# Kernel optimization log

Measured on AMD Instinct MI355X. Metric: run time of the kernel, lower is better.

The kernel has to match this reference:

```python
import jax, jax.numpy as jnp
import numpy as np

N, E = 50000, 800000
IN_CH, OUT_CH, MSG_DIM, TIME_DIM = 128, 128, 128, 128
HEADS = 2
HEAD_C = OUT_CH // HEADS  # 64
EDGE_DIM = MSG_DIM + TIME_DIM  # 256


def setup_inputs() -> dict:
    key = jax.random.key(0)
    ks = jax.random.split(key, 16)
    s = 0.05
    return {
        "x": jax.random.normal(ks[0], (N, IN_CH), jnp.float32),
        "last_update": jax.random.uniform(ks[1], (N,), jnp.float32),
        "t": jax.random.uniform(ks[2], (E,), jnp.float32),
        "msg": jax.random.normal(ks[3], (E, MSG_DIM), jnp.float32),
        "edge_index": jax.random.randint(ks[4], (2, E), 0, N, jnp.int64),
        # TimeEncoder: Linear(1, TIME_DIM) then cos
        "W_time": jax.random.normal(ks[5], (1, TIME_DIM), jnp.float32) * s,
        "b_time": jax.random.normal(ks[6], (TIME_DIM,), jnp.float32) * s,
        # TransformerConv linears (stored [in, out])
        "Wq": jax.random.normal(ks[7], (IN_CH, OUT_CH), jnp.float32) * s,
        "bq": jax.random.normal(ks[8], (OUT_CH,), jnp.float32) * s,
        "Wk": jax.random.normal(ks[9], (IN_CH, OUT_CH), jnp.float32) * s,
        "bk": jax.random.normal(ks[10], (OUT_CH,), jnp.float32) * s,
        "Wv": jax.random.normal(ks[11], (IN_CH, OUT_CH), jnp.float32) * s,
        "bv": jax.random.normal(ks[12], (OUT_CH,), jnp.float32) * s,
        "We": jax.random.normal(ks[13], (EDGE_DIM, OUT_CH), jnp.float32) * s,  # lin_edge, no bias
        "Ws": jax.random.normal(ks[14], (IN_CH, OUT_CH), jnp.float32) * s,  # lin_skip (root weight)
        "bs": jax.random.normal(ks[15], (OUT_CH,), jnp.float32) * s,
    }


def reference(x, last_update, t, msg, edge_index, W_time, b_time,
              Wq, bq, Wk, bk, Wv, bv, We, Ws, bs):
    src, dst = edge_index[0], edge_index[1]
    # --- temporal edge features ---
    rel_t = last_update[src] - t                      # [E]
    rel_t_enc = jnp.cos(rel_t[:, None] * W_time[0] + b_time)  # [E, TIME_DIM]
    edge_attr = jnp.concatenate([rel_t_enc, msg], axis=-1)    # [E, EDGE_DIM]
    # --- TransformerConv (heads=2, concat=True, root_weight=True, eval: no dropout) ---
    q = (x @ Wq + bq).reshape(N, HEADS, HEAD_C)[dst]   # [E,H,C] query at destination
    k = (x @ Wk + bk).reshape(N, HEADS, HEAD_C)[src]   # [E,H,C] key at source
    v = (x @ Wv + bv).reshape(N, HEADS, HEAD_C)[src]   # [E,H,C]
    e = (edge_attr @ We).reshape(E, HEADS, HEAD_C)     # [E,H,C]
    k = k + e
    alpha = jnp.sum(q * k, axis=-1) / jnp.sqrt(jnp.asarray(HEAD_C, x.dtype))  # [E,H]
    # segment softmax over edges grouped by destination node
    m = jax.ops.segment_max(alpha, dst, num_segments=N)       # [N,H]
    p = jnp.exp(alpha - m[dst])                               # [E,H]
    denom = jax.ops.segment_sum(p, dst, num_segments=N)       # [N,H]
    attn = p / denom[dst]                                     # [E,H]
    out_e = attn[:, :, None] * (v + e)                        # [E,H,C]
    out = jax.ops.segment_sum(out_e, dst, num_segments=N).reshape(N, HEADS * HEAD_C)
    return out + x @ Ws + bs
```

## Files before the change

### kernel.cpp

```cpp
#include <hip/hip_runtime.h>
#include <math.h>

#define N_NODES 50000
#define N_EDGES 800000
#define CH 128
#define GDIM 512

__global__ __launch_bounds__(256) void build_M_kernel(
    const float* __restrict__ Wq, const float* __restrict__ We,
    float* __restrict__ M)
{
    __shared__ float wq[CH];
    const int i = blockIdx.x, t = threadIdx.x;
    if (t < CH) wq[t] = Wq[i * CH + t];
    __syncthreads();
    #pragma unroll
    for (int rep = 0; rep < 2; ++rep) {
        int f  = rep * 256 + t;
        int h  = f >> 8, jj = f & 255;
        const float* wer = We + (size_t)jj * CH + h * 64;
        const float* wqr = wq + h * 64;
        float s = 0.f;
        #pragma unroll 8
        for (int c = 0; c < 64; ++c) s = fmaf(wqr[c], wer[c], s);
        M[(size_t)i * GDIM + f] = s;
    }
}

__global__ void build_gbias_kernel(const float* __restrict__ bq,
                                   const float* __restrict__ We,
                                   float* __restrict__ gb)
{
    int f = blockIdx.x * 256 + threadIdx.x;
    int h = f >> 8, jj = f & 255;
    float s = 0.f;
    #pragma unroll 8
    for (int c = 0; c < 64; ++c)
        s = fmaf(bq[h * 64 + c], We[(size_t)jj * CH + h * 64 + c], s);
    gb[f] = s;
}

__global__ __launch_bounds__(256) void node_linear_kernel(
    const float* __restrict__ x,
    const float* __restrict__ Wq, const float* __restrict__ bq,
    const float* __restrict__ Wk, const float* __restrict__ bk,
    const float* __restrict__ Wv, const float* __restrict__ bv,
    const float* __restrict__ Ws, const float* __restrict__ bs,
    const float* __restrict__ M,  const float* __restrict__ gb,
    float* __restrict__ Q, float* __restrict__ K,
    float* __restrict__ V, float* __restrict__ S, float* __restrict__ G)
{
    __shared__ float xs[64][CH];
    const int t  = threadIdx.x;
    const int n0 = blockIdx.x * 64;

    #pragma unroll
    for (int r = 0; r < 8; ++r) {
        int flat4 = r * 256 + t;
        int row   = flat4 >> 5;
        int c4    = (flat4 & 31) * 4;
        int gr    = n0 + row; if (gr >= N_NODES) gr = N_NODES - 1;
        *(float4*)&xs[row][c4] = *(const float4*)&x[(size_t)gr * CH + c4];
    }
    __syncthreads();

    const int tx = t & 31, ey = t >> 5;
    const int c0 = tx * 4, e0 = ey * 8;

    const float* Wp[8]   = {Wq, Wk, Wv, Ws, M, M + 128, M + 256, M + 384};
    const int    wstr[8] = {CH, CH, CH, CH, GDIM, GDIM, GDIM, GDIM};
    const float* Bp[8]   = {bq, bk, bv, bs, gb, gb + 128, gb + 256, gb + 384};
    float*       Op[8]   = {Q, K, V, S, G, G + 128, G + 256, G + 384};
    const int    ostr[8] = {CH, CH, CH, CH, GDIM, GDIM, GDIM, GDIM};

    #pragma unroll
    for (int m = 0; m < 8; ++m) {
        const float* W = Wp[m];
        const int ws_ = wstr[m];
        float4 acc[8];
        #pragma unroll
        for (int i = 0; i < 8; ++i) acc[i] = make_float4(0.f, 0.f, 0.f, 0.f);
        for (int j = 0; j < CH; ++j) {
            float4 w = *(const float4*)&W[(size_t)j * ws_ + c0];
            #pragma unroll
            for (int i = 0; i < 8; ++i) {
                float a = xs[e0 + i][j];
                acc[i].x = fmaf(a, w.x, acc[i].x);
                acc[i].y = fmaf(a, w.y, acc[i].y);
                acc[i].z = fmaf(a, w.z, acc[i].z);
                acc[i].w = fmaf(a, w.w, acc[i].w);
            }
        }
        float4 b4 = *(const float4*)&Bp[m][c0];
        float* O  = Op[m];
        const int os = ostr[m];
        #pragma unroll
        for (int i = 0; i < 8; ++i) {
            int n = n0 + e0 + i;
            if (n < N_NODES) {
                float4 r = make_float4(acc[i].x + b4.x, acc[i].y + b4.y,
                                       acc[i].z + b4.z, acc[i].w + b4.w);
                *(float4*)&O[(size_t)n * os + c0] = r;
            }
        }
    }
}

__global__ void hist_kernel(const int* __restrict__ ei, int* __restrict__ cnt)
{
    int e = blockIdx.x * 256 + threadIdx.x;
    atomicAdd(&cnt[ei[N_EDGES + e]], 1);
}

__global__ __launch_bounds__(1024) void scan_kernel(
    const int* __restrict__ cnt, int* __restrict__ base, int* __restrict__ cursor)
{
    __shared__ int ssum[1024];
    const int t = threadIdx.x;
    const int STRIP = 49;
    const int s0 = t * STRIP;
    int sum = 0;
    for (int i = 0; i < STRIP; ++i) {
        int idx = s0 + i;
        sum += (idx < N_NODES) ? cnt[idx] : 0;
    }
    ssum[t] = sum;
    __syncthreads();
    for (int off = 1; off < 1024; off <<= 1) {
        int v = (t >= off) ? ssum[t - off] : 0;
        __syncthreads();
        ssum[t] += v;
        __syncthreads();
    }
    int run = (t > 0) ? ssum[t - 1] : 0;
    for (int i = 0; i < STRIP; ++i) {
        int idx = s0 + i;
        if (idx < N_NODES) {
            base[idx] = run; cursor[idx] = run;
            run += cnt[idx];
        }
    }
    if (t == 1023) base[N_NODES] = ssum[1023];
}

__global__ void scatter_kernel(const int* __restrict__ ei,
                               const float* __restrict__ last_update,
                               const float* __restrict__ t_arr,
                               int* __restrict__ cursor,
                               int2* __restrict__ sedge,
                               float* __restrict__ srt)
{
    int e = blockIdx.x * 256 + threadIdx.x;
    int s = ei[e];
    int d = ei[N_EDGES + e];
    int pos = atomicAdd(&cursor[d], 1);
    sedge[pos] = make_int2(s, e);
    srt[pos] = last_update[s] - t_arr[e];
}

__device__ __forceinline__ float wave_allsum(float p) {
    p += __int_as_float(__builtin_amdgcn_update_dpp(
            0, __float_as_int(p), 0xB1, 0xF, 0xF, true));
    p += __int_as_float(__builtin_amdgcn_update_dpp(
            0, __float_as_int(p), 0x4E, 0xF, 0xF, true));
    p += __int_as_float(__builtin_amdgcn_update_dpp(
            0, __float_as_int(p), 0x141, 0xF, 0xF, true));
    p += __int_as_float(__builtin_amdgcn_update_dpp(
            0, __float_as_int(p), 0x140, 0xF, 0xF, true));
    p += __int_as_float(__builtin_amdgcn_ds_swizzle(__float_as_int(p), 0x401F));
    p += __shfl_xor(p, 32);
    return p;
}

__global__ __launch_bounds__(256) void gather_attn_kernel(
    const float* __restrict__ msg,
    const float* __restrict__ W_time,
    const float* __restrict__ b_time,
    const float* __restrict__ We,
    const float* __restrict__ Q, const float* __restrict__ K,
    const float* __restrict__ V, const float* __restrict__ S,
    const float* __restrict__ G,
    const int* __restrict__ base,
    const int2* __restrict__ sedge,
    const float* __restrict__ srt,
    float* __restrict__ out)
{
    __shared__ float wabuf[4][GDIM];
    __shared__ float nvbuf[4][CH];
    __shared__ float dsh[4][2];
    __shared__ int   degsh[4];
    const int wv = threadIdx.x >> 6;
    const int j  = threadIdx.x & 63;
    const int n  = blockIdx.x * 4 + wv;

    const float q0 = Q[(size_t)n * CH + j];
    const float q1 = Q[(size_t)n * CH + 64 + j];
    const float* gn = G + (size_t)n * GDIM + j;
    const float g00 = gn[0],   g01 = gn[64],  g02 = gn[128], g03 = gn[192];
    const float g10 = gn[256], g11 = gn[320], g12 = gn[384], g13 = gn[448];
    const float wt0 = W_time[j], wt1 = W_time[64 + j];
    const float bt0 = b_time[j], bt1 = b_time[64 + j];

    float wa00 = 0.f, wa01 = 0.f, wa02 = 0.f, wa03 = 0.f;
    float wa10 = 0.f, wa11 = 0.f, wa12 = 0.f, wa13 = 0.f;
    float nv0 = 0.f, nv1 = 0.f, den0 = 0.f, den1 = 0.f;

    const int b0 = base[n], b1 = base[n + 1];
    int i = b0;

    for (; i + 2 <= b1; i += 2) {
        const int2  seA = sedge[i];
        const int2  seB = sedge[i + 1];
        const float rtA = srt[i];
        const float rtB = srt[i + 1];
        const float* mA  = msg + (size_t)seA.y * CH;
        const float* mB  = msg + (size_t)seB.y * CH;
        const float* kpA = K   + (size_t)seA.x * CH;
        const float* kpB = K   + (size_t)seB.x * CH;
        const float* vpA = V   + (size_t)seA.x * CH;
        const float* vpB = V   + (size_t)seB.x * CH;

        float ea2A = mA[j],      ea3A = mA[64 + j];
        float ea2B = mB[j],      ea3B = mB[64 + j];
        float k0A  = kpA[j],     k1A  = kpA[64 + j];
        float k0B  = kpB[j],     k1B  = kpB[64 + j];
        float v0A  = vpA[j],     v1A  = vpA[64 + j];
        float v0B  = vpB[j],     v1B  = vpB[64 + j];

        float ea0A = __cosf(fmaf(rtA, wt0, bt0));
        float ea1A = __cosf(fmaf(rtA, wt1, bt1));
        float ea0B = __cosf(fmaf(rtB, wt0, bt0));
        float ea1B = __cosf(fmaf(rtB, wt1, bt1));

        float pA0 = fmaf(q0, k0A, fmaf(ea0A, g00, fmaf(ea1A, g01, fmaf(ea2A, g02, ea3A * g03))));
        float pA1 = fmaf(q1, k1A, fmaf(ea0A, g10, fmaf(ea1A, g11, fmaf(ea2A, g12, ea3A * g13))));
        float pB0 = fmaf(q0, k0B, fmaf(ea0B, g00, fmaf(ea1B, g01, fmaf(ea2B, g02, ea3B * g03))));
        float pB1 = fmaf(q1, k1B, fmaf(ea0B, g10, fmaf(ea1B, g11, fmaf(ea2B, g12, ea3B * g13))));

        pA0 = wave_allsum(pA0);
        pA1 = wave_allsum(pA1);
        pB0 = wave_allsum(pB0);
        pB1 = wave_allsum(pB1);

        pA0 = __expf(pA0 * 0.125f);
        pA1 = __expf(pA1 * 0.125f);
        pB0 = __expf(pB0 * 0.125f);
        pB1 = __expf(pB1 * 0.125f);

        den0 += pA0; den0 += pB0;
        den1 += pA1; den1 += pB1;
        wa00 = fmaf(pA0, ea0A, wa00); wa00 = fmaf(pB0, ea0B, wa00);
        wa01 = fmaf(pA0, ea1A, wa01); wa01 = fmaf(pB0, ea1B, wa01);
        wa02 = fmaf(pA0, ea2A, wa02); wa02 = fmaf(pB0, ea2B, wa02);
        wa03 = fmaf(pA0, ea3A, wa03); wa03 = fmaf(pB0, ea3B, wa03);
        wa10 = fmaf(pA1, ea0A, wa10); wa10 = fmaf(pB1, ea0B, wa10);
        wa11 = fmaf(pA1, ea1A, wa11); wa11 = fmaf(pB1, ea1B, wa11);
        wa12 = fmaf(pA1, ea2A, wa12); wa12 = fmaf(pB1, ea2B, wa12);
        wa13 = fmaf(pA1, ea3A, wa13); wa13 = fmaf(pB1, ea3B, wa13);
        nv0  = fmaf(pA0, v0A, nv0);   nv0  = fmaf(pB0, v0B, nv0);
        nv1  = fmaf(pA1, v1A, nv1);   nv1  = fmaf(pB1, v1B, nv1);
    }

    if (i < b1) {
        const int2  se = sedge[i];
        const float rt = srt[i];
        const float* m  = msg + (size_t)se.y * CH;
        const float* kp = K   + (size_t)se.x * CH;
        const float* vp = V   + (size_t)se.x * CH;
        float ea2 = m[j],  ea3 = m[64 + j];
        float k0  = kp[j], k1  = kp[64 + j];
        float v0  = vp[j], v1  = vp[64 + j];
        float ea0 = __cosf(fmaf(rt, wt0, bt0));
        float ea1 = __cosf(fmaf(rt, wt1, bt1));

        float p0 = fmaf(q0, k0, fmaf(ea0, g00, fmaf(ea1, g01, fmaf(ea2, g02, ea3 * g03))));
        float p1 = fmaf(q1, k1, fmaf(ea0, g10, fmaf(ea1, g11, fmaf(ea2, g12, ea3 * g13))));
        p0 = wave_allsum(p0);
        p1 = wave_allsum(p1);
        p0 = __expf(p0 * 0.125f);
        p1 = __expf(p1 * 0.125f);

        den0 += p0; den1 += p1;
        wa00 = fmaf(p0, ea0, wa00); wa01 = fmaf(p0, ea1, wa01);
        wa02 = fmaf(p0, ea2, wa02); wa03 = fmaf(p0, ea3, wa03);
        wa10 = fmaf(p1, ea0, wa10); wa11 = fmaf(p1, ea1, wa11);
        wa12 = fmaf(p1, ea2, wa12); wa13 = fmaf(p1, ea3, wa13);
        nv0  = fmaf(p0, v0, nv0);
        nv1  = fmaf(p1, v1, nv1);
    }

    wabuf[wv][j]       = wa00; wabuf[wv][64 + j]  = wa01;
    wabuf[wv][128 + j] = wa02; wabuf[wv][192 + j] = wa03;
    wabuf[wv][256 + j] = wa10; wabuf[wv][320 + j] = wa11;
    wabuf[wv][384 + j] = wa12; wabuf[wv][448 + j] = wa13;
    nvbuf[wv][j]      = nv0;
    nvbuf[wv][64 + j] = nv1;
    if (j == 0) {
        dsh[wv][0] = den0; dsh[wv][1] = den1;
        degsh[wv]  = b1 - b0;
    }
    __syncthreads();

    const int col = threadIdx.x & 127;
    const int pr  = threadIdx.x >> 7;
    const int h   = col >> 6;
    const int nA  = 2 * pr, nB = 2 * pr + 1;
    const int wo  = h * 256;

    float aA = 0.f, aB = 0.f;
    #pragma unroll 8
    for (int jj = 0; jj < 256; ++jj) {
        float w = We[(size_t)jj * CH + col];
        aA = fmaf(wabuf[nA][wo + jj], w, aA);
        aB = fmaf(wabuf[nB][wo + jj], w, aB);
    }

    {
        int node = blockIdx.x * 4 + nA;
        float r = (degsh[nA] > 0) ? (nvbuf[nA][col] + aA) / dsh[nA][h] : 0.f;
        out[(size_t)node * CH + col] = r + S[(size_t)node * CH + col];
    }
    {
        int node = blockIdx.x * 4 + nB;
        float r = (degsh[nB] > 0) ? (nvbuf[nB][col] + aB) / dsh[nB][h] : 0.f;
        out[(size_t)node * CH + col] = r + S[(size_t)node * CH + col];
    }
}

extern "C" void kernel_launch(void* const* d_in, const int* in_sizes, int n_in,
                              void* d_out, int out_size, void* d_ws, size_t ws_size,
                              hipStream_t stream) {
    const float* x           = (const float*)d_in[0];
    const float* last_update = (const float*)d_in[1];
    const float* t           = (const float*)d_in[2];
    const float* msg         = (const float*)d_in[3];
    const int*   edge_index  = (const int*)d_in[4];
    const float* W_time      = (const float*)d_in[5];
    const float* b_time      = (const float*)d_in[6];
    const float* Wq = (const float*)d_in[7];
    const float* bq = (const float*)d_in[8];
    const float* Wk = (const float*)d_in[9];
    const float* bk = (const float*)d_in[10];
    const float* Wv = (const float*)d_in[11];
    const float* bv = (const float*)d_in[12];
    const float* We = (const float*)d_in[13];
    const float* Ws = (const float*)d_in[14];
    const float* bs = (const float*)d_in[15];
    float* out = (float*)d_out;

    float* ws = (float*)d_ws;
    const size_t NC = (size_t)N_NODES * CH;
    float* Q  = ws;
    float* K  = Q + NC;
    float* V  = K + NC;
    float* S  = V + NC;
    float* G  = S + NC;
    float* M  = G + (size_t)N_NODES * GDIM;
    float* gb = M + (size_t)CH * GDIM;
    int* cnt    = (int*)(gb + GDIM);
    int* base   = cnt + N_NODES;
    int* cursor = base + N_NODES + 1;
    size_t off = (size_t)((char*)(cursor + N_NODES) - (char*)d_ws);
    off = (off + 7) & ~(size_t)7;
    int2*  sedge = (int2*)((char*)d_ws + off);
    float* srt   = (float*)(sedge + N_EDGES);

    hipMemsetAsync(cnt, 0, (size_t)N_NODES * sizeof(int), stream);

    build_M_kernel<<<CH, 256, 0, stream>>>(Wq, We, M);
    build_gbias_kernel<<<2, 256, 0, stream>>>(bq, We, gb);

    node_linear_kernel<<<(N_NODES + 63) / 64, 256, 0, stream>>>(
        x, Wq, bq, Wk, bk, Wv, bv, Ws, bs, M, gb, Q, K, V, S, G);

    hist_kernel<<<N_EDGES / 256, 256, 0, stream>>>(edge_index, cnt);
    scan_kernel<<<1, 1024, 0, stream>>>(cnt, base, cursor);
    scatter_kernel<<<N_EDGES / 256, 256, 0, stream>>>(
        edge_index, last_update, t, cursor, sedge, srt);

    gather_attn_kernel<<<N_NODES / 4, 256, 0, stream>>>(
        msg, W_time, b_time, We,
        Q, K, V, S, G, base, sedge, srt, out);
}
```

Baseline: 1.167 ms.

## Process four edges per wave with float4 half-wave lanes and packed edge records

Result: slower. 1.217 ms (+4.3%).

```diff
diff --git a/kernel.cpp b/kernel.cpp
--- a/kernel.cpp
+++ b/kernel.cpp
@@ -7,13 +7,16 @@
 #define GDIM 512
 
 __global__ __launch_bounds__(256) void build_M_kernel(
-    const float* __restrict__ Wq, const float* __restrict__ We,
-    float* __restrict__ M)
+    const float* __restrict__ Wq, const float* __restrict__ bq,
+    const float* __restrict__ We,
+    float* __restrict__ M, float* __restrict__ gb)
 {
     __shared__ float wq[CH];
     const int i = blockIdx.x, t = threadIdx.x;
-    if (t < CH) wq[t] = Wq[i * CH + t];
+    const float* srcrow = (i < CH) ? (Wq + (size_t)i * CH) : bq;
+    if (t < CH) wq[t] = srcrow[t];
     __syncthreads();
+    float* orow = (i < CH) ? (M + (size_t)i * GDIM) : gb;
     #pragma unroll
     for (int rep = 0; rep < 2; ++rep) {
         int f  = rep * 256 + t;
@@ -23,21 +26,8 @@
         float s = 0.f;
         #pragma unroll 8
         for (int c = 0; c < 64; ++c) s = fmaf(wqr[c], wer[c], s);
-        M[(size_t)i * GDIM + f] = s;
-    }
-}
-
-__global__ void build_gbias_kernel(const float* __restrict__ bq,
-                                   const float* __restrict__ We,
-                                   float* __restrict__ gb)
-{
-    int f = blockIdx.x * 256 + threadIdx.x;
-    int h = f >> 8, jj = f & 255;
-    float s = 0.f;
-    #pragma unroll 8
-    for (int c = 0; c < 64; ++c)
-        s = fmaf(bq[h * 64 + c], We[(size_t)jj * CH + h * 64 + c], s);
-    gb[f] = s;
+        orow[f] = s;
+    }
 }
 
 __global__ __launch_bounds__(256) void node_linear_kernel(
@@ -147,18 +137,17 @@
                                const float* __restrict__ last_update,
                                const float* __restrict__ t_arr,
                                int* __restrict__ cursor,
-                               int2* __restrict__ sedge,
-                               float* __restrict__ srt)
+                               int4* __restrict__ sedge)
 {
     int e = blockIdx.x * 256 + threadIdx.x;
     int s = ei[e];
     int d = ei[N_EDGES + e];
+    float rt = last_update[s] - t_arr[e];
     int pos = atomicAdd(&cursor[d], 1);
-    sedge[pos] = make_int2(s, e);
-    srt[pos] = last_update[s] - t_arr[e];
-}
-
-__device__ __forceinline__ float wave_allsum(float p) {
+    sedge[pos] = make_int4(s, e, __float_as_int(rt), 0);
+}
+
+__device__ __forceinline__ float half_allsum(float p) {
     p += __int_as_float(__builtin_amdgcn_update_dpp(
             0, __float_as_int(p), 0xB1, 0xF, 0xF, true));
     p += __int_as_float(__builtin_amdgcn_update_dpp(
@@ -168,11 +157,22 @@
     p += __int_as_float(__builtin_amdgcn_update_dpp(
             0, __float_as_int(p), 0x140, 0xF, 0xF, true));
     p += __int_as_float(__builtin_amdgcn_ds_swizzle(__float_as_int(p), 0x401F));
-    p += __shfl_xor(p, 32);
     return p;
 }
 
-__global__ __launch_bounds__(256) void gather_attn_kernel(
+__device__ __forceinline__ float dot4(float4 a, float4 b) {
+    return fmaf(a.x, b.x, fmaf(a.y, b.y, fmaf(a.z, b.z, a.w * b.w)));
+}
+
+#define FMA4(acc, s, v) \
+    acc.x = fmaf(s, v.x, acc.x); acc.y = fmaf(s, v.y, acc.y); \
+    acc.z = fmaf(s, v.z, acc.z); acc.w = fmaf(s, v.w, acc.w)
+
+#define XC4(v) \
+    v.x += __shfl_xor(v.x, 32); v.y += __shfl_xor(v.y, 32); \
+    v.z += __shfl_xor(v.z, 32); v.w += __shfl_xor(v.w, 32)
+
+__global__ __launch_bounds__(256, 4) void gather_attn_kernel(
     const float* __restrict__ msg,
     const float* __restrict__ W_time,
     const float* __restrict__ b_time,
@@ -181,123 +181,111 @@
     const float* __restrict__ V, const float* __restrict__ S,
     const float* __restrict__ G,
     const int* __restrict__ base,
-    const int2* __restrict__ sedge,
-    const float* __restrict__ srt,
+    const int4* __restrict__ sedge,
     float* __restrict__ out)
 {
     __shared__ float wabuf[4][GDIM];
     __shared__ float nvbuf[4][CH];
     __shared__ float dsh[4][2];
     __shared__ int   degsh[4];
-    const int wv = threadIdx.x >> 6;
-    const int j  = threadIdx.x & 63;
-    const int n  = blockIdx.x * 4 + wv;
-
-    const float q0 = Q[(size_t)n * CH + j];
-    const float q1 = Q[(size_t)n * CH + 64 + j];
-    const float* gn = G + (size_t)n * GDIM + j;
-    const float g00 = gn[0],   g01 = gn[64],  g02 = gn[128], g03 = gn[192];
-    const float g10 = gn[256], g11 = gn[320], g12 = gn[384], g13 = gn[448];
-    const float wt0 = W_time[j], wt1 = W_time[64 + j];
-    const float bt0 = b_time[j], bt1 = b_time[64 + j];
-
-    float wa00 = 0.f, wa01 = 0.f, wa02 = 0.f, wa03 = 0.f;
-    float wa10 = 0.f, wa11 = 0.f, wa12 = 0.f, wa13 = 0.f;
-    float nv0 = 0.f, nv1 = 0.f, den0 = 0.f, den1 = 0.f;
+
+    const int wv   = threadIdx.x >> 6;
+    const int lane = threadIdx.x & 63;
+    const int h32  = lane >> 5;
+    const int l    = lane & 31;
+    const int c0   = l * 4;
+    const float mh0 = (l < 16) ? 1.f : 0.f;
+    const int n = blockIdx.x * 4 + wv;
+
+    const float4 q4  = *(const float4*)&Q[(size_t)n * CH + c0];
+    const float* gp  = G + (size_t)n * GDIM;
+    const float4 gt0 = *(const float4*)&gp[c0];
+    const float4 gm0 = *(const float4*)&gp[128 + c0];
+    const float4 gt1 = *(const float4*)&gp[256 + c0];
+    const float4 gm1 = *(const float4*)&gp[384 + c0];
+    const float4 wt4 = *(const float4*)&W_time[c0];
+    const float4 bt4 = *(const float4*)&b_time[c0];
+
+    float4 waT0 = {0,0,0,0}, waM0 = {0,0,0,0};
+    float4 waT1 = {0,0,0,0}, waM1 = {0,0,0,0};
+    float4 nv4  = {0,0,0,0};
+    float den0 = 0.f, den1 = 0.f;
 
     const int b0 = base[n], b1 = base[n + 1];
-    int i = b0;
-
-    for (; i + 2 <= b1; i += 2) {
-        const int2  seA = sedge[i];
-        const int2  seB = sedge[i + 1];
-        const float rtA = srt[i];
-        const float rtB = srt[i + 1];
-        const float* mA  = msg + (size_t)seA.y * CH;
-        const float* mB  = msg + (size_t)seB.y * CH;
-        const float* kpA = K   + (size_t)seA.x * CH;
-        const float* kpB = K   + (size_t)seB.x * CH;
-        const float* vpA = V   + (size_t)seA.x * CH;
-        const float* vpB = V   + (size_t)seB.x * CH;
-
-        float ea2A = mA[j],      ea3A = mA[64 + j];
-        float ea2B = mB[j],      ea3B = mB[64 + j];
-        float k0A  = kpA[j],     k1A  = kpA[64 + j];
-        float k0B  = kpB[j],     k1B  = kpB[64 + j];
-        float v0A  = vpA[j],     v1A  = vpA[64 + j];
-        float v0B  = vpB[j],     v1B  = vpB[64 + j];
-
-        float ea0A = __cosf(fmaf(rtA, wt0, bt0));
-        float ea1A = __cosf(fmaf(rtA, wt1, bt1));
-        float ea0B = __cosf(fmaf(rtB, wt0, bt0));
-        float ea1B = __cosf(fmaf(rtB, wt1, bt1));
-
-        float pA0 = fmaf(q0, k0A, fmaf(ea0A, g00, fmaf(ea1A, g01, fmaf(ea2A, g02, ea3A * g03))));
-        float pA1 = fmaf(q1, k1A, fmaf(ea0A, g10, fmaf(ea1A, g11, fmaf(ea2A, g12, ea3A * g13))));
-        float pB0 = fmaf(q0, k0B, fmaf(ea0B, g00, fmaf(ea1B, g01, fmaf(ea2B, g02, ea3B * g03))));
-        float pB1 = fmaf(q1, k1B, fmaf(ea0B, g10, fmaf(ea1B, g11, fmaf(ea2B, g12, ea3B * g13))));
-
-        pA0 = wave_allsum(pA0);
-        pA1 = wave_allsum(pA1);
-        pB0 = wave_allsum(pB0);
-        pB1 = wave_allsum(pB1);
-
-        pA0 = __expf(pA0 * 0.125f);
-        pA1 = __expf(pA1 * 0.125f);
-        pB0 = __expf(pB0 * 0.125f);
-        pB1 = __expf(pB1 * 0.125f);
-
-        den0 += pA0; den0 += pB0;
-        den1 += pA1; den1 += pB1;
-        wa00 = fmaf(pA0, ea0A, wa00); wa00 = fmaf(pB0, ea0B, wa00);
-        wa01 = fmaf(pA0, ea1A, wa01); wa01 = fmaf(pB0, ea1B, wa01);
-        wa02 = fmaf(pA0, ea2A, wa02); wa02 = fmaf(pB0, ea2B, wa02);
-        wa03 = fmaf(pA0, ea3A, wa03); wa03 = fmaf(pB0, ea3B, wa03);
-        wa10 = fmaf(pA1, ea0A, wa10); wa10 = fmaf(pB1, ea0B, wa10);
-        wa11 = fmaf(pA1, ea1A, wa11); wa11 = fmaf(pB1, ea1B, wa11);
-        wa12 = fmaf(pA1, ea2A, wa12); wa12 = fmaf(pB1, ea2B, wa12);
-        wa13 = fmaf(pA1, ea3A, wa13); wa13 = fmaf(pB1, ea3B, wa13);
-        nv0  = fmaf(pA0, v0A, nv0);   nv0  = fmaf(pB0, v0B, nv0);
-        nv1  = fmaf(pA1, v1A, nv1);   nv1  = fmaf(pB1, v1B, nv1);
-    }
-
-    if (i < b1) {
-        const int2  se = sedge[i];
-        const float rt = srt[i];
-        const float* m  = msg + (size_t)se.y * CH;
-        const float* kp = K   + (size_t)se.x * CH;
-        const float* vp = V   + (size_t)se.x * CH;
-        float ea2 = m[j],  ea3 = m[64 + j];
-        float k0  = kp[j], k1  = kp[64 + j];
-        float v0  = vp[j], v1  = vp[64 + j];
-        float ea0 = __cosf(fmaf(rt, wt0, bt0));
-        float ea1 = __cosf(fmaf(rt, wt1, bt1));
-
-        float p0 = fmaf(q0, k0, fmaf(ea0, g00, fmaf(ea1, g01, fmaf(ea2, g02, ea3 * g03))));
-        float p1 = fmaf(q1, k1, fmaf(ea0, g10, fmaf(ea1, g11, fmaf(ea2, g12, ea3 * g13))));
-        p0 = wave_allsum(p0);
-        p1 = wave_allsum(p1);
-        p0 = __expf(p0 * 0.125f);
-        p1 = __expf(p1 * 0.125f);
-
-        den0 += p0; den1 += p1;
-        wa00 = fmaf(p0, ea0, wa00); wa01 = fmaf(p0, ea1, wa01);
-        wa02 = fmaf(p0, ea2, wa02); wa03 = fmaf(p0, ea3, wa03);
-        wa10 = fmaf(p1, ea0, wa10); wa11 = fmaf(p1, ea1, wa11);
-        wa12 = fmaf(p1, ea2, wa12); wa13 = fmaf(p1, ea3, wa13);
-        nv0  = fmaf(p0, v0, nv0);
-        nv1  = fmaf(p1, v1, nv1);
-    }
-
-    wabuf[wv][j]       = wa00; wabuf[wv][64 + j]  = wa01;
-    wabuf[wv][128 + j] = wa02; wabuf[wv][192 + j] = wa03;
-    wabuf[wv][256 + j] = wa10; wabuf[wv][320 + j] = wa11;
-    wabuf[wv][384 + j] = wa12; wabuf[wv][448 + j] = wa13;
-    nvbuf[wv][j]      = nv0;
-    nvbuf[wv][64 + j] = nv1;
-    if (j == 0) {
-        dsh[wv][0] = den0; dsh[wv][1] = den1;
-        degsh[wv]  = b1 - b0;
+
+    for (int i = b0; i < b1; i += 4) {
+        const int  iA = i + h32;
+        const int  iB = i + 2 + h32;
+        const bool vA = iA < b1;
+        const bool vB = iB < b1;
+        const int4 eA = sedge[vA ? iA : b1 - 1];
+        const int4 eB = sedge[vB ? iB : b1 - 1];
+        const float rtA = __int_as_float(eA.z);
+        const float rtB = __int_as_float(eB.z);
+
+        const float4 mA  = *(const float4*)&msg[(size_t)eA.y * CH + c0];
+        const float4 kA  = *(const float4*)&K  [(size_t)eA.x * CH + c0];
+        const float4 vA4 = *(const float4*)&V  [(size_t)eA.x * CH + c0];
+        const float4 mB  = *(const float4*)&msg[(size_t)eB.y * CH + c0];
+        const float4 kB  = *(const float4*)&K  [(size_t)eB.x * CH + c0];
+        const float4 vB4 = *(const float4*)&V  [(size_t)eB.x * CH + c0];
+
+        float4 etA, etB;
+        etA.x = __cosf(fmaf(rtA, wt4.x, bt4.x));
+        etA.y = __cosf(fmaf(rtA, wt4.y, bt4.y));
+        etA.z = __cosf(fmaf(rtA, wt4.z, bt4.z));
+        etA.w = __cosf(fmaf(rtA, wt4.w, bt4.w));
+        etB.x = __cosf(fmaf(rtB, wt4.x, bt4.x));
+        etB.y = __cosf(fmaf(rtB, wt4.y, bt4.y));
+        etB.z = __cosf(fmaf(rtB, wt4.z, bt4.z));
+        etB.w = __cosf(fmaf(rtB, wt4.w, bt4.w));
+
+        const float qkA = dot4(q4, kA);
+        const float qkB = dot4(q4, kB);
+
+        float uA = fmaf(mh0,       qkA, dot4(etA, gt0) + dot4(mA, gm0));
+        float wA = fmaf(1.f - mh0, qkA, dot4(etA, gt1) + dot4(mA, gm1));
+        float uB = fmaf(mh0,       qkB, dot4(etB, gt0) + dot4(mB, gm0));
+        float wB = fmaf(1.f - mh0, qkB, dot4(etB, gt1) + dot4(mB, gm1));
+
+        uA = half_allsum(uA);
+        wA = half_allsum(wA);
+        uB = half_allsum(uB);
+        wB = half_allsum(wB);
+
+        const float p0A = vA ? __expf(uA * 0.125f) : 0.f;
+        const float p1A = vA ? __expf(wA * 0.125f) : 0.f;
+        const float p0B = vB ? __expf(uB * 0.125f) : 0.f;
+        const float p1B = vB ? __expf(wB * 0.125f) : 0.f;
+
+        den0 += p0A + p0B;
+        den1 += p1A + p1B;
+
+        FMA4(waT0, p0A, etA); FMA4(waT0, p0B, etB);
+        FMA4(waM0, p0A, mA);  FMA4(waM0, p0B, mB);
+        FMA4(waT1, p1A, etA); FMA4(waT1, p1B, etB);
+        FMA4(waM1, p1A, mA);  FMA4(waM1, p1B, mB);
+
+        const float pA = (l < 16) ? p0A : p1A;
+        const float pB = (l < 16) ? p0B : p1B;
+        FMA4(nv4, pA, vA4);
+        FMA4(nv4, pB, vB4);
+    }
+
+    XC4(waT0); XC4(waM0); XC4(waT1); XC4(waM1); XC4(nv4);
+    den0 += __shfl_xor(den0, 32);
+    den1 += __shfl_xor(den1, 32);
+
+    if (h32 == 0) {
+        *(float4*)&wabuf[wv][c0]       = waT0;
+        *(float4*)&wabuf[wv][128 + c0] = waM0;
+        *(float4*)&wabuf[wv][256 + c0] = waT1;
+        *(float4*)&wabuf[wv][384 + c0] = waM1;
+        *(float4*)&nvbuf[wv][c0]       = nv4;
+        if (l == 0) {
+            dsh[wv][0] = den0; dsh[wv][1] = den1;
+            degsh[wv]  = b1 - b0;
+        }
     }
     __syncthreads();
 
@@ -361,14 +349,12 @@
     int* base   = cnt + N_NODES;
     int* cursor = base + N_NODES + 1;
     size_t off = (size_t)((char*)(cursor + N_NODES) - (char*)d_ws);
-    off = (off + 7) & ~(size_t)7;
-    int2*  sedge = (int2*)((char*)d_ws + off);
-    float* srt   = (float*)(sedge + N_EDGES);
+    off = (off + 15) & ~(size_t)15;
+    int4* sedge = (int4*)((char*)d_ws + off);
 
     hipMemsetAsync(cnt, 0, (size_t)N_NODES * sizeof(int), stream);
 
-    build_M_kernel<<<CH, 256, 0, stream>>>(Wq, We, M);
-    build_gbias_kernel<<<2, 256, 0, stream>>>(bq, We, gb);
+    build_M_kernel<<<CH + 1, 256, 0, stream>>>(Wq, bq, We, M, gb);
 
     node_linear_kernel<<<(N_NODES + 63) / 64, 256, 0, stream>>>(
         x, Wq, bq, Wk, bk, Wv, bv, Ws, bs, M, gb, Q, K, V, S, G);
@@ -376,9 +362,9 @@
     hist_kernel<<<N_EDGES / 256, 256, 0, stream>>>(edge_index, cnt);
     scan_kernel<<<1, 1024, 0, stream>>>(cnt, base, cursor);
     scatter_kernel<<<N_EDGES / 256, 256, 0, stream>>>(
-        edge_index, last_update, t, cursor, sedge, srt);
+        edge_index, last_update, t, cursor, sedge);
 
     gather_attn_kernel<<<N_NODES / 4, 256, 0, stream>>>(
         msg, W_time, b_time, We,
-        Q, K, V, S, G, base, sedge, srt, out);
-}
+        Q, K, V, S, G, base, sedge, out);
+}
```
